# Optimization experiments

Measured on AMD Instinct MI355X. Metric: run time of the kernel, lower is better.

Reference implementation:

```python
import jax, jax.numpy as jnp
import numpy as np

EMBED_DIM = 2048
NUM_HEADS = 16
LATENT_DIM = 512
HEAD_DIM = EMBED_DIM // NUM_HEADS


def setup_inputs() -> dict:
    key = jax.random.key(0)
    ks = jax.random.split(key, 9)
    s = 0.02
    x = jax.random.normal(ks[0], (2, 2048, EMBED_DIM), dtype=jnp.float32)
    # torch Linear weights stored as [out, in]
    q_w = jax.random.normal(ks[1], (EMBED_DIM, EMBED_DIM), jnp.float32) * s
    q_b = jax.random.normal(ks[2], (EMBED_DIM,), jnp.float32) * s
    kvd_w = jax.random.normal(ks[3], (LATENT_DIM, EMBED_DIM), jnp.float32) * s
    kvd_b = jax.random.normal(ks[4], (LATENT_DIM,), jnp.float32) * s
    kvu_w = jax.random.normal(ks[5], (EMBED_DIM * 2, LATENT_DIM), jnp.float32) * s
    kvu_b = jax.random.normal(ks[6], (EMBED_DIM * 2,), jnp.float32) * s
    out_w = jax.random.normal(ks[7], (EMBED_DIM, EMBED_DIM), jnp.float32) * s
    out_b = jax.random.normal(ks[8], (EMBED_DIM,), jnp.float32) * s
    return {"x": x, "q_w": q_w, "q_b": q_b, "kvd_w": kvd_w, "kvd_b": kvd_b,
            "kvu_w": kvu_w, "kvu_b": kvu_b, "out_w": out_w, "out_b": out_b}


def reference(x, q_w, q_b, kvd_w, kvd_b, kvu_w, kvu_b, out_w, out_b):
    b, s, _ = x.shape
    q = x @ q_w.T + q_b                      # [b,s,E]
    latent = x @ kvd_w.T + kvd_b             # [b,s,L]
    kv = latent @ kvu_w.T + kvu_b            # [b,s,2E]
    k, v = kv[..., :EMBED_DIM], kv[..., EMBED_DIM:]
    def heads(t):
        return t.reshape(b, s, NUM_HEADS, HEAD_DIM).transpose(0, 2, 1, 3)  # [b,h,s,d]
    qh, kh, vh = heads(q), heads(k), heads(v)
    scores = jnp.einsum('bhqd,bhkd->bhqk', qh, kh) / jnp.sqrt(jnp.float32(HEAD_DIM))
    attn = jax.nn.softmax(scores, axis=-1)
    out = jnp.einsum('bhqk,bhkd->bhqd', attn, vh)
    out = out.transpose(0, 2, 1, 3).reshape(b, s, EMBED_DIM)
    return out @ out_w.T + out_b
```

## Files before the change

### kernel.cpp

```cpp
#include <hip/hip_runtime.h>

typedef unsigned short u16;
typedef __attribute__((ext_vector_type(8))) __bf16 bf16x8;
typedef __attribute__((ext_vector_type(8))) unsigned short u16x8;
typedef __attribute__((ext_vector_type(4))) float f32x4;
typedef __attribute__((ext_vector_type(16))) float f32x16;

#define BK 32

__device__ __forceinline__ u16 f32_to_bf16(float f) {
  unsigned int u = __builtin_bit_cast(unsigned int, f);
  u += 0x7fffu + ((u >> 16) & 1u);
  return (u16)(u >> 16);
}

__global__ __launch_bounds__(256) void cvt_bf16(const float* __restrict__ in,
                                                u16* __restrict__ out, int n) {
  int i = (blockIdx.x * 256 + threadIdx.x) * 4;
  if (i >= n) return;
  float4 v = *(const float4*)(in + i);
  ushort4 o;
  o.x = f32_to_bf16(v.x);
  o.y = f32_to_bf16(v.y);
  o.z = f32_to_bf16(v.z);
  o.w = f32_to_bf16(v.w);
  *(ushort4*)(out + i) = o;
}

__device__ __forceinline__ void gemm_core(const u16* __restrict__ A,
                                          const u16* __restrict__ B, int K,
                                          u16* As, u16* Bs, f32x4 acc[4][4]) {
  const int tid = threadIdx.x;
  const int w = tid >> 6, lane = tid & 63;
  const int wm = (w >> 1) << 6, wn = (w & 1) << 6;
  const int quad = lane >> 4, l15 = lane & 15;
  const int bm = blockIdx.y, bn = blockIdx.x;

  const int a0 = (bm * 128 + (tid >> 2)) * K + (tid & 3) * 8;
  const int a1 = a0 + 64 * K;
  const int b0 = (bn * 128 + (tid >> 2)) * K + (tid & 3) * 8;
  const int b1 = b0 + 64 * K;

  for (int k0 = 0; k0 < K; k0 += BK) {
    u16x8 va0 = *(const u16x8*)(A + a0 + k0);
    u16x8 va1 = *(const u16x8*)(A + a1 + k0);
    u16x8 vb0 = *(const u16x8*)(B + b0 + k0);
    u16x8 vb1 = *(const u16x8*)(B + b1 + k0);
    __syncthreads();
    *(u16x8*)(As + tid * 8) = va0;
    *(u16x8*)(As + (256 + tid) * 8) = va1;
    *(u16x8*)(Bs + tid * 8) = vb0;
    *(u16x8*)(Bs + (256 + tid) * 8) = vb1;
    __syncthreads();
    bf16x8 af[4], bf[4];
#pragma unroll
    for (int i = 0; i < 4; i++)
      af[i] = *(const bf16x8*)(As + (wm + i * 16 + l15) * BK + quad * 8);
#pragma unroll
    for (int j = 0; j < 4; j++)
      bf[j] = *(const bf16x8*)(Bs + (wn + j * 16 + l15) * BK + quad * 8);
#pragma unroll
    for (int i = 0; i < 4; i++)
#pragma unroll
      for (int j = 0; j < 4; j++)
        acc[i][j] =
            __builtin_amdgcn_mfma_f32_16x16x32_bf16(af[i], bf[j], acc[i][j], 0, 0, 0);
  }
}

__global__ __launch_bounds__(256) void gemm_bf16out(const u16* __restrict__ A,
                                                    const u16* __restrict__ B,
                                                    const float* __restrict__ bias,
                                                    u16* __restrict__ C, int K, int N) {
  __shared__ __align__(16) u16 As[128 * BK];
  __shared__ __align__(16) u16 Bs[128 * BK];
  f32x4 acc[4][4];
  const f32x4 z = {0.f, 0.f, 0.f, 0.f};
#pragma unroll
  for (int i = 0; i < 4; i++)
#pragma unroll
    for (int j = 0; j < 4; j++) acc[i][j] = z;
  gemm_core(A, B, K, As, Bs, acc);

  const int tid = threadIdx.x;
  const int w = tid >> 6, lane = tid & 63;
  const int wm = (w >> 1) << 6, wn = (w & 1) << 6;
  const int quad = lane >> 4, l15 = lane & 15;
  const int row0 = blockIdx.y * 128 + wm + quad * 4;
  const int col0 = blockIdx.x * 128 + wn + l15;
#pragma unroll
  for (int i = 0; i < 4; i++)
#pragma unroll
    for (int j = 0; j < 4; j++) {
      int col = col0 + j * 16;
      float bv = bias[col];
#pragma unroll
      for (int r = 0; r < 4; r++) {
        int row = row0 + i * 16 + r;
        C[(size_t)row * N + col] = f32_to_bf16(acc[i][j][r] + bv);
      }
    }
}

__global__ __launch_bounds__(256) void gemm_f32out(const u16* __restrict__ A,
                                                   const u16* __restrict__ B,
                                                   const float* __restrict__ bias,
                                                   float* __restrict__ C, int K, int N) {
  __shared__ __align__(16) u16 As[128 * BK];
  __shared__ __align__(16) u16 Bs[128 * BK];
  f32x4 acc[4][4];
  const f32x4 z = {0.f, 0.f, 0.f, 0.f};
#pragma unroll
  for (int i = 0; i < 4; i++)
#pragma unroll
    for (int j = 0; j < 4; j++) acc[i][j] = z;
  gemm_core(A, B, K, As, Bs, acc);

  const int tid = threadIdx.x;
  const int w = tid >> 6, lane = tid & 63;
  const int wm = (w >> 1) << 6, wn = (w & 1) << 6;
  const int quad = lane >> 4, l15 = lane & 15;
  const int row0 = blockIdx.y * 128 + wm + quad * 4;
  const int col0 = blockIdx.x * 128 + wn + l15;
#pragma unroll
  for (int i = 0; i < 4; i++)
#pragma unroll
    for (int j = 0; j < 4; j++) {
      int col = col0 + j * 16;
      float bv = bias[col];
#pragma unroll
      for (int r = 0; r < 4; r++) {
        int row = row0 + i * 16 + r;
        C[(size_t)row * N + col] = acc[i][j][r] + bv;
      }
    }
}

__global__ __launch_bounds__(256) void gemm_kv(const u16* __restrict__ A,
                                               const u16* __restrict__ B,
                                               const float* __restrict__ bias,
                                               u16* __restrict__ Khat,
                                               u16* __restrict__ Vt, int K) {
  __shared__ __align__(16) u16 As[128 * BK];
  __shared__ __align__(16) u16 Bs[128 * BK];
  f32x4 acc[4][4];
  const f32x4 z = {0.f, 0.f, 0.f, 0.f};
#pragma unroll
  for (int i = 0; i < 4; i++)
#pragma unroll
    for (int j = 0; j < 4; j++) acc[i][j] = z;
  gemm_core(A, B, K, As, Bs, acc);

  const int tid = threadIdx.x;
  const int w = tid >> 6, lane = tid & 63;
  const int wm = (w >> 1) << 6, wn = (w & 1) << 6;
  const int quad = lane >> 4, l15 = lane & 15;
  const int row0 = blockIdx.y * 128 + wm + quad * 4;
  const int col0 = blockIdx.x * 128 + wn + l15;
#pragma unroll
  for (int i = 0; i < 4; i++)
#pragma unroll
    for (int j = 0; j < 4; j++) {
      int n = col0 + j * 16;
      float bv = bias[n];
#pragma unroll
      for (int r = 0; r < 4; r++) {
        int row = row0 + i * 16 + r;
        int bb = row >> 11, s = row & 2047;
        u16 val = f32_to_bf16(acc[i][j][r] + bv);
        if (n < 2048) {
          int h = n >> 7, d = n & 127;
          Khat[((size_t)(bb * 16 + h) * 2048 + s) * 128 + d] = val;
        } else {
          int h = (n - 2048) >> 7, d = n & 127;
          Vt[((size_t)(bb * 16 + h) * 128 + d) * 2048 + s] = val;
        }
      }
    }
}

__global__ __launch_bounds__(256) void attn_kernel(const u16* __restrict__ Q,
                                                   const u16* __restrict__ Khat,
                                                   const u16* __restrict__ Vt,
                                                   u16* __restrict__ O) {
  __shared__ __align__(16) u16 Ks[64 * 136];
  __shared__ __align__(16) u16 Vs[128 * 72];
  __shared__ __align__(16) u16 Ps[4 * 32 * 72];

  const int tid = threadIdx.x;
  const int w = tid >> 6, lane = tid & 63;
  const int l31 = lane & 31, half = lane >> 5;
  const int qt = blockIdx.x & 15;
  const int h = (blockIdx.x >> 4) & 15;
  const int b = blockIdx.x >> 8;
  const int bh = b * 16 + h;
  const float SC = 0.08838834764831845f * 1.4426950408889634f;

  bf16x8 qf[8];
  {
    const u16* qrow = Q + (size_t)(b * 2048 + qt * 128 + w * 32 + l31) * 2048 +
                      h * 128 + half * 8;
#pragma unroll
    for (int kc = 0; kc < 8; kc++) qf[kc] = *(const bf16x8*)(qrow + kc * 16);
  }

  f32x16 oacc[4];
#pragma unroll
  for (int nt = 0; nt < 4; nt++)
#pragma unroll
    for (int r = 0; r < 16; r++) oacc[nt][r] = 0.f;
  float lsum[16];
#pragma unroll
  for (int r = 0; r < 16; r++) lsum[r] = 0.f;

  const u16* Kg = Khat + (size_t)bh * 2048 * 128;
  const u16* Vg = Vt + (size_t)bh * 128 * 2048;
  u16* Pw = Ps + w * 32 * 72;

  for (int key0 = 0; key0 < 2048; key0 += 64) {
    u16x8 kv[4], vv[4];
#pragma unroll
    for (int it = 0; it < 4; it++) {
      int slot = it * 256 + tid;
      int kr = slot >> 4, c = slot & 15;
      kv[it] = *(const u16x8*)(Kg + (size_t)(key0 + kr) * 128 + c * 8);
    }
#pragma unroll
    for (int it = 0; it < 4; it++) {
      int slot = it * 256 + tid;
      int d = slot >> 3, c = slot & 7;
      vv[it] = *(const u16x8*)(Vg + (size_t)d * 2048 + key0 + c * 8);
    }
    __syncthreads();
#pragma unroll
    for (int it = 0; it < 4; it++) {
      int slot = it * 256 + tid;
      int kr = slot >> 4, c = slot & 15;
      *(u16x8*)(Ks + kr * 136 + c * 8) = kv[it];
    }
#pragma unroll
    for (int it = 0; it < 4; it++) {
      int slot = it * 256 + tid;
      int d = slot >> 3, c = slot & 7;
      *(u16x8*)(Vs + d * 72 + c * 8) = vv[it];
    }
    __syncthreads();

    f32x16 sacc[2];
#pragma unroll
    for (int ct = 0; ct < 2; ct++)
#pragma unroll
      for (int r = 0; r < 16; r++) sacc[ct][r] = 0.f;
#pragma unroll
    for (int ct = 0; ct < 2; ct++)
#pragma unroll
      for (int kc = 0; kc < 8; kc++) {
        bf16x8 kf =
            *(const bf16x8*)(Ks + (ct * 32 + l31) * 136 + kc * 16 + half * 8);
        sacc[ct] =
            __builtin_amdgcn_mfma_f32_32x32x16_bf16(qf[kc], kf, sacc[ct], 0, 0, 0);
      }

#pragma unroll
    for (int ct = 0; ct < 2; ct++)
#pragma unroll
      for (int r = 0; r < 16; r++) {
        float e = exp2f(sacc[ct][r] * SC);
        lsum[r] += e;
        int ridx = (r & 3) + 8 * (r >> 2) + 4 * half;
        Pw[ridx * 72 + ct * 32 + l31] = f32_to_bf16(e);
      }

    bf16x8 pf[4];
#pragma unroll
    for (int kc = 0; kc < 4; kc++)
      pf[kc] = *(const bf16x8*)(Pw + l31 * 72 + kc * 16 + half * 8);
#pragma unroll
    for (int nt = 0; nt < 4; nt++)
#pragma unroll
      for (int kc = 0; kc < 4; kc++) {
        bf16x8 vf =
            *(const bf16x8*)(Vs + (nt * 32 + l31) * 72 + kc * 16 + half * 8);
        oacc[nt] =
            __builtin_amdgcn_mfma_f32_32x32x16_bf16(pf[kc], vf, oacc[nt], 0, 0, 0);
      }
  }

#pragma unroll
  for (int r = 0; r < 16; r++) {
    float s = lsum[r];
    s += __shfl_xor(s, 1);
    s += __shfl_xor(s, 2);
    s += __shfl_xor(s, 4);
    s += __shfl_xor(s, 8);
    s += __shfl_xor(s, 16);
    lsum[r] = 1.0f / s;
  }

#pragma unroll
  for (int nt = 0; nt < 4; nt++)
#pragma unroll
    for (int r = 0; r < 16; r++) {
      int ridx = (r & 3) + 8 * (r >> 2) + 4 * half;
      int row = b * 2048 + qt * 128 + w * 32 + ridx;
      int col = h * 128 + nt * 32 + l31;
      O[(size_t)row * 2048 + col] = f32_to_bf16(oacc[nt][r] * lsum[r]);
    }
}

extern "C" void kernel_launch(void* const* d_in, const int* in_sizes, int n_in,
                              void* d_out, int out_size, void* d_ws, size_t ws_size,
                              hipStream_t stream) {
  (void)in_sizes; (void)n_in; (void)out_size; (void)ws_size;
  const float* x     = (const float*)d_in[0];
  const float* q_w   = (const float*)d_in[1];
  const float* q_b   = (const float*)d_in[2];
  const float* kvd_w = (const float*)d_in[3];
  const float* kvd_b = (const float*)d_in[4];
  const float* kvu_w = (const float*)d_in[5];
  const float* kvu_b = (const float*)d_in[6];
  const float* out_w = (const float*)d_in[7];
  const float* out_b = (const float*)d_in[8];
  float* out = (float*)d_out;

  char* p = (char*)d_ws;
  u16* X    = (u16*)(p + 0);
  u16* W1   = (u16*)(p + (size_t)16 * 1024 * 1024);
  u16* W2   = (u16*)(p + (size_t)24 * 1024 * 1024);
  u16* Qb   = (u16*)(p + (size_t)26 * 1024 * 1024);
  u16* Lat  = (u16*)(p + (size_t)42 * 1024 * 1024);
  u16* Khat = (u16*)(p + (size_t)46 * 1024 * 1024);
  u16* Vt   = (u16*)(p + (size_t)62 * 1024 * 1024);
  u16* AO   = (u16*)(p + (size_t)78 * 1024 * 1024);

  cvt_bf16<<<dim3(8192), dim3(256), 0, stream>>>(x, X, 8388608);
  cvt_bf16<<<dim3(4096), dim3(256), 0, stream>>>(q_w, W1, 4194304);
  cvt_bf16<<<dim3(1024), dim3(256), 0, stream>>>(kvd_w, W2, 1048576);

  gemm_bf16out<<<dim3(16, 32), dim3(256), 0, stream>>>(X, W1, q_b, Qb, 2048, 2048);
  gemm_bf16out<<<dim3(4, 32), dim3(256), 0, stream>>>(X, W2, kvd_b, Lat, 2048, 512);

  cvt_bf16<<<dim3(2048), dim3(256), 0, stream>>>(kvu_w, W1, 2097152);
  gemm_kv<<<dim3(32, 32), dim3(256), 0, stream>>>(Lat, W1, kvu_b, Khat, Vt, 512);

  cvt_bf16<<<dim3(4096), dim3(256), 0, stream>>>(out_w, X, 4194304);
  attn_kernel<<<dim3(512), dim3(256), 0, stream>>>(Qb, Khat, Vt, AO);
  gemm_f32out<<<dim3(16, 32), dim3(256), 0, stream>>>(AO, X, out_b, out, 2048, 2048);
}
```

Baseline: 445.2 us.

## Double-buffer GEMM LDS tiles and merge Q and latent projections into one launch

The shared GEMM core now double-buffers its LDS tiles. It prefetches the next K slice into registers while the MFMAs run on the current buffer, then writes it to the other buffer, which removes one barrier per iteration. The separate Q projection and KV-down projection GEMMs are merged into one 20x32 grid launch that picks weights, bias and output per block column. This should overlap global loads with compute and fill the GPU better than the small 4x32 latent launch alone, at the cost of doubled LDS per block.

```diff
diff --git a/kernel.cpp b/kernel.cpp
--- a/kernel.cpp
+++ b/kernel.cpp
@@ -7,6 +7,7 @@
 typedef __attribute__((ext_vector_type(16))) float f32x16;
 
 #define BK 32
+#define TILE_ELEMS (128 * BK)
 
 __device__ __forceinline__ u16 f32_to_bf16(float f) {
   unsigned int u = __builtin_bit_cast(unsigned int, f);
@@ -27,67 +28,92 @@
   *(ushort4*)(out + i) = o;
 }
 
-__device__ __forceinline__ void gemm_core(const u16* __restrict__ A,
-                                          const u16* __restrict__ B, int K,
+__device__ __forceinline__ void gemm_core(const u16* __restrict__ A_tile,
+                                          const u16* __restrict__ B_tile, int K,
                                           u16* As, u16* Bs, f32x4 acc[4][4]) {
   const int tid = threadIdx.x;
   const int w = tid >> 6, lane = tid & 63;
   const int wm = (w >> 1) << 6, wn = (w & 1) << 6;
   const int quad = lane >> 4, l15 = lane & 15;
-  const int bm = blockIdx.y, bn = blockIdx.x;
-
-  const int a0 = (bm * 128 + (tid >> 2)) * K + (tid & 3) * 8;
-  const int a1 = a0 + 64 * K;
-  const int b0 = (bn * 128 + (tid >> 2)) * K + (tid & 3) * 8;
-  const int b1 = b0 + 64 * K;
-
+
+  const u16* Ap = A_tile + (tid >> 2) * K + (tid & 3) * 8;
+  const u16* Bp = B_tile + (tid >> 2) * K + (tid & 3) * 8;
+
+  u16x8 ra0 = *(const u16x8*)Ap;
+  u16x8 ra1 = *(const u16x8*)(Ap + 64 * K);
+  u16x8 rb0 = *(const u16x8*)Bp;
+  u16x8 rb1 = *(const u16x8*)(Bp + 64 * K);
+  *(u16x8*)(As + tid * 8) = ra0;
+  *(u16x8*)(As + (256 + tid) * 8) = ra1;
+  *(u16x8*)(Bs + tid * 8) = rb0;
+  *(u16x8*)(Bs + (256 + tid) * 8) = rb1;
+
+  int p = 0;
   for (int k0 = 0; k0 < K; k0 += BK) {
-    u16x8 va0 = *(const u16x8*)(A + a0 + k0);
-    u16x8 va1 = *(const u16x8*)(A + a1 + k0);
-    u16x8 vb0 = *(const u16x8*)(B + b0 + k0);
-    u16x8 vb1 = *(const u16x8*)(B + b1 + k0);
+    const int kn = (k0 + BK < K) ? (k0 + BK) : 0;
+    ra0 = *(const u16x8*)(Ap + kn);
+    ra1 = *(const u16x8*)(Ap + 64 * K + kn);
+    rb0 = *(const u16x8*)(Bp + kn);
+    rb1 = *(const u16x8*)(Bp + 64 * K + kn);
     __syncthreads();
-    *(u16x8*)(As + tid * 8) = va0;
-    *(u16x8*)(As + (256 + tid) * 8) = va1;
-    *(u16x8*)(Bs + tid * 8) = vb0;
-    *(u16x8*)(Bs + (256 + tid) * 8) = vb1;
-    __syncthreads();
+    const u16* Asr = As + p * TILE_ELEMS;
+    const u16* Bsr = Bs + p * TILE_ELEMS;
     bf16x8 af[4], bf[4];
 #pragma unroll
     for (int i = 0; i < 4; i++)
-      af[i] = *(const bf16x8*)(As + (wm + i * 16 + l15) * BK + quad * 8);
+      af[i] = *(const bf16x8*)(Asr + (wm + i * 16 + l15) * BK + quad * 8);
 #pragma unroll
     for (int j = 0; j < 4; j++)
-      bf[j] = *(const bf16x8*)(Bs + (wn + j * 16 + l15) * BK + quad * 8);
+      bf[j] = *(const bf16x8*)(Bsr + (wn + j * 16 + l15) * BK + quad * 8);
 #pragma unroll
     for (int i = 0; i < 4; i++)
 #pragma unroll
       for (int j = 0; j < 4; j++)
         acc[i][j] =
             __builtin_amdgcn_mfma_f32_16x16x32_bf16(af[i], bf[j], acc[i][j], 0, 0, 0);
+    const int pn = p ^ 1;
+    u16* Asw = As + pn * TILE_ELEMS;
+    u16* Bsw = Bs + pn * TILE_ELEMS;
+    *(u16x8*)(Asw + tid * 8) = ra0;
+    *(u16x8*)(Asw + (256 + tid) * 8) = ra1;
+    *(u16x8*)(Bsw + tid * 8) = rb0;
+    *(u16x8*)(Bsw + (256 + tid) * 8) = rb1;
+    p = pn;
   }
 }
 
-__global__ __launch_bounds__(256) void gemm_bf16out(const u16* __restrict__ A,
-                                                    const u16* __restrict__ B,
-                                                    const float* __restrict__ bias,
-                                                    u16* __restrict__ C, int K, int N) {
-  __shared__ __align__(16) u16 As[128 * BK];
-  __shared__ __align__(16) u16 Bs[128 * BK];
+__global__ __launch_bounds__(256) void gemm_qlat(const u16* __restrict__ X,
+                                                 const u16* __restrict__ QW,
+                                                 const u16* __restrict__ KVDW,
+                                                 const float* __restrict__ q_b,
+                                                 const float* __restrict__ kvd_b,
+                                                 u16* __restrict__ Qb,
+                                                 u16* __restrict__ Lat) {
+  __shared__ __align__(16) u16 As[2 * TILE_ELEMS];
+  __shared__ __align__(16) u16 Bs[2 * TILE_ELEMS];
+  const int bn = blockIdx.x, bm = blockIdx.y;
+  const bool isq = bn < 16;
+  const u16* B_tile = isq ? QW + (size_t)bn * 128 * 2048
+                          : KVDW + (size_t)(bn - 16) * 128 * 2048;
   f32x4 acc[4][4];
   const f32x4 z = {0.f, 0.f, 0.f, 0.f};
 #pragma unroll
   for (int i = 0; i < 4; i++)
 #pragma unroll
     for (int j = 0; j < 4; j++) acc[i][j] = z;
-  gemm_core(A, B, K, As, Bs, acc);
+  gemm_core(X + (size_t)bm * 128 * 2048, B_tile, 2048, As, Bs, acc);
+
+  const float* bias = isq ? q_b : kvd_b;
+  u16* C = isq ? Qb : Lat;
+  const int N = isq ? 2048 : 512;
+  const int colbase = (isq ? bn : bn - 16) * 128;
 
   const int tid = threadIdx.x;
   const int w = tid >> 6, lane = tid & 63;
   const int wm = (w >> 1) << 6, wn = (w & 1) << 6;
   const int quad = lane >> 4, l15 = lane & 15;
-  const int row0 = blockIdx.y * 128 + wm + quad * 4;
-  const int col0 = blockIdx.x * 128 + wn + l15;
+  const int row0 = bm * 128 + wm + quad * 4;
+  const int col0 = colbase + wn + l15;
 #pragma unroll
   for (int i = 0; i < 4; i++)
 #pragma unroll
@@ -106,15 +132,16 @@
                                                    const u16* __restrict__ B,
                                                    const float* __restrict__ bias,
                                                    float* __restrict__ C, int K, int N) {
-  __shared__ __align__(16) u16 As[128 * BK];
-  __shared__ __align__(16) u16 Bs[128 * BK];
+  __shared__ __align__(16) u16 As[2 * TILE_ELEMS];
+  __shared__ __align__(16) u16 Bs[2 * TILE_ELEMS];
   f32x4 acc[4][4];
   const f32x4 z = {0.f, 0.f, 0.f, 0.f};
 #pragma unroll
   for (int i = 0; i < 4; i++)
 #pragma unroll
     for (int j = 0; j < 4; j++) acc[i][j] = z;
-  gemm_core(A, B, K, As, Bs, acc);
+  gemm_core(A + (size_t)blockIdx.y * 128 * K, B + (size_t)blockIdx.x * 128 * K, K,
+            As, Bs, acc);
 
   const int tid = threadIdx.x;
   const int w = tid >> 6, lane = tid & 63;
@@ -141,15 +168,16 @@
                                                const float* __restrict__ bias,
                                                u16* __restrict__ Khat,
                                                u16* __restrict__ Vt, int K) {
-  __shared__ __align__(16) u16 As[128 * BK];
-  __shared__ __align__(16) u16 Bs[128 * BK];
+  __shared__ __align__(16) u16 As[2 * TILE_ELEMS];
+  __shared__ __align__(16) u16 Bs[2 * TILE_ELEMS];
   f32x4 acc[4][4];
   const f32x4 z = {0.f, 0.f, 0.f, 0.f};
 #pragma unroll
   for (int i = 0; i < 4; i++)
 #pragma unroll
     for (int j = 0; j < 4; j++) acc[i][j] = z;
-  gemm_core(A, B, K, As, Bs, acc);
+  gemm_core(A + (size_t)blockIdx.y * 128 * K, B + (size_t)blockIdx.x * 128 * K, K,
+            As, Bs, acc);
 
   const int tid = threadIdx.x;
   const int w = tid >> 6, lane = tid & 63;
@@ -337,8 +365,7 @@
   cvt_bf16<<<dim3(4096), dim3(256), 0, stream>>>(q_w, W1, 4194304);
   cvt_bf16<<<dim3(1024), dim3(256), 0, stream>>>(kvd_w, W2, 1048576);
 
-  gemm_bf16out<<<dim3(16, 32), dim3(256), 0, stream>>>(X, W1, q_b, Qb, 2048, 2048);
-  gemm_bf16out<<<dim3(4, 32), dim3(256), 0, stream>>>(X, W2, kvd_b, Lat, 2048, 512);
+  gemm_qlat<<<dim3(20, 32), dim3(256), 0, stream>>>(X, W1, W2, q_b, kvd_b, Qb, Lat);
 
   cvt_bf16<<<dim3(2048), dim3(256), 0, stream>>>(kvu_w, W1, 2097152);
   gemm_kv<<<dim3(32, 32), dim3(256), 0, stream>>>(Lat, W1, kvu_b, Khat, Vt, 512);
```

Measured after the change: 411.4 us. -7.6%, faster.
